# Kernel tuning notes

Measured on AMD Instinct MI355X. Metric: run time of the kernel, lower is better.

The kernel has to match this reference:

```python
import jax, jax.numpy as jnp
import numpy as np

EPSILON = 0.05


def _l2_normalize(x, axis=1, eps=1e-12):
    return x / jnp.maximum(jnp.linalg.norm(x, axis=axis, keepdims=True), eps)


def _pairwise_euclidean_distance(a, b):
    # [N, d], [K, d] -> [N, K] euclidean distances (torch.cdist semantics)
    sq = (jnp.sum(a * a, axis=1)[:, None]
          + jnp.sum(b * b, axis=1)[None, :]
          - 2.0 * (a @ b.T))
    return jnp.sqrt(jnp.maximum(sq, 1e-12))


def _sinkhorn(out, epsilon):
    # Faithful to the original: the loop body never updates Q, so the result
    # is a single row-then-column normalization regardless of `iterations`.
    Q = jnp.exp(out / epsilon).T              # [K, B]
    K, B = Q.shape
    Q = Q / jnp.sum(Q)
    Q1 = Q / jnp.sum(Q, axis=1, keepdims=True) / K
    Q2 = Q1 / jnp.sum(Q1, axis=0, keepdims=True) / B
    return (Q2 * B).T                          # [B, K]


def _cross_entropy(x1, x2):
    return -jnp.mean(jnp.sum(x1 * jnp.log(x2), axis=1))


def setup_inputs() -> dict:
    key = jax.random.key(0)
    k1, k2, k3 = jax.random.split(key, 3)
    two_bsz, d, K = 32768, 256, 1024
    return {
        "z": jax.random.normal(k1, (two_bsz, d), dtype=jnp.float32),
        "p": jax.random.normal(k2, (two_bsz, d), dtype=jnp.float32),
        "centers": jax.random.normal(k3, (K, d), dtype=jnp.float32),
    }


def reference(z, p, centers):
    z = _l2_normalize(z, axis=1)
    p = _l2_normalize(p, axis=1)
    c = _l2_normalize(centers, axis=1)

    bsz = z.shape[0] // 2
    z1, z2 = z[:bsz], z[bsz:]
    p1, p2 = p[:bsz], p[bsz:]

    za_1 = _sinkhorn(_pairwise_euclidean_distance(z1, c), EPSILON)
    za_2 = _sinkhorn(_pairwise_euclidean_distance(z2, c), EPSILON)
    pa_1 = _sinkhorn(_pairwise_euclidean_distance(p1, c), EPSILON)
    pa_2 = _sinkhorn(_pairwise_euclidean_distance(p2, c), EPSILON)

    # cls_use_both_views = True
    return (_cross_entropy(za_1, pa_1) + _cross_entropy(za_1, pa_2)
            + _cross_entropy(za_2, pa_1) + _cross_entropy(za_2, pa_2)) / 4.0
```

## Files before the change

kernel.cpp:

```cpp
#include <hip/hip_runtime.h>
#include <math.h>

#define BH  16384
#define B2  32768
#define DIM 256
#define KC  1024

typedef __bf16 bf16x8 __attribute__((ext_vector_type(8)));
typedef float  f32x4  __attribute__((ext_vector_type(4)));

__device__ __forceinline__ unsigned short f2bf(float f) {
  unsigned int u = __float_as_uint(f);
  u += 0x7FFFu + ((u >> 16) & 1u);
  return (unsigned short)(u >> 16);
}

__device__ __forceinline__ float vsqrt(float x) {
  float r; asm("v_sqrt_f32 %0, %1" : "=v"(r) : "v"(x)); return r;
}

__device__ __forceinline__ void gld_lds16(const void* g, void* l) {
  __builtin_amdgcn_global_load_lds(
      (const __attribute__((address_space(1))) void*)g,
      (__attribute__((address_space(3))) void*)l, 16, 0, 0);
}

__global__ void norm_rows_kernel(const float* __restrict__ z,
                                 const float* __restrict__ p,
                                 const float* __restrict__ c,
                                 unsigned short* __restrict__ Xn,
                                 unsigned short* __restrict__ Cn,
                                 float* __restrict__ colsum,
                                 float* __restrict__ out) {
  if (blockIdx.x < 16) colsum[blockIdx.x * 256 + threadIdx.x] = 0.0f;
  if (blockIdx.x == 16 && threadIdx.x == 0) out[0] = 0.0f;

  int wave = threadIdx.x >> 6;
  int lane = threadIdx.x & 63;
  int row  = blockIdx.x * 4 + wave;
  const float* src; unsigned short* dst; int r;
  if (row < B2)        { src = z; dst = Xn; r = row; }
  else if (row < 2*B2) { src = p; dst = Xn + (size_t)B2 * DIM; r = row - B2; }
  else                 { src = c; dst = Cn; r = row - 2*B2; }
  float4 v = *reinterpret_cast<const float4*>(src + (size_t)r * DIM + lane * 4);
  float ss = v.x*v.x + v.y*v.y + v.z*v.z + v.w*v.w;
  #pragma unroll
  for (int m = 1; m < 64; m <<= 1) ss += __shfl_xor(ss, m);
  float inv = 1.0f / fmaxf(vsqrt(ss), 1e-12f);
  ushort4 o;
  o.x = f2bf(v.x * inv); o.y = f2bf(v.y * inv);
  o.z = f2bf(v.z * inv); o.w = f2bf(v.w * inv);
  *reinterpret_cast<ushort4*>(dst + (size_t)r * DIM + lane * 4) = o;
}

__global__ void fin_logC_kernel(const float* __restrict__ colsum,
                                float* __restrict__ logC) {
  int i = blockIdx.x * 256 + threadIdx.x;
  if (i < 4 * KC) logC[i] = 40.0f + __logf(colsum[i]);
}

__global__ __launch_bounds__(256, 2)
void gemm_s_kernel(const unsigned short* __restrict__ XA,
                   const unsigned short* __restrict__ Cn,
                   float* __restrict__ colsum,
                   unsigned char* __restrict__ S) {
  __shared__ __align__(16) char lds[65536 + 4096];
  float* lut4 = (float*)(lds + 65536);
  const int id  = blockIdx.x;
  const int xcd = id & 7, idx = id >> 3;
  const int wk  = xcd * 128 + idx;
  const int panel = wk >> 3, col = wk & 7;
  const int tm0 = panel * 128, tn0 = col * 128;

  const int tid  = threadIdx.x;
  const int lane = tid & 63;
  const int wid  = tid >> 6;
  const int wm   = wid >> 1, wn = wid & 1;
  const int l15  = lane & 15, l4 = lane >> 4;
  const int slot = tid & 3;

  int arow[4], acs[4];
  #pragma unroll
  for (int it = 0; it < 4; ++it) {
    int sl = it * 256 + tid;
    int r = sl >> 3, c = sl & 7;
    arow[it] = r;
    acs[it]  = c ^ (r & 7);
  }
  const char* Abase = (const char*)XA + (size_t)tm0 * 512;
  const char* Bbase = (const char*)Cn + (size_t)tn0 * 512;

  auto stage = [&](int t) {
    const int mat = t >> 2;
    const int bk  = t & 3;
    const int b   = t & 1;
    const char* ab = Abase + ((size_t)mat << 23);
    #pragma unroll
    for (int it = 0; it < 4; ++it) {
      gld_lds16(ab + (size_t)arow[it] * 512 + bk * 128 + acs[it] * 16,
                lds + b * 16384 + (it * 256 + tid) * 16);
      gld_lds16(Bbase + (size_t)arow[it] * 512 + bk * 128 + acs[it] * 16,
                lds + 32768 + b * 16384 + (it * 256 + tid) * 16);
    }
  };

  if (tid < 256) {
    float d = ((float)tid - 127.5f) * (1.0f / 255.0f);
    float L = 20.0f * vsqrt(2.0f - 2.0f * d);
    float v = __expf(L - 40.0f);
    ((float4*)lut4)[tid] = (float4){v, v, v, v};
  }

  f32x4 acc[4][4];
  stage(0);
  __syncthreads();

  for (int t = 0; t < 16; ++t) {
    if (t < 15) stage(t + 1);
    const int b  = t & 1;
    const int mat = t >> 2, bk = t & 3;

    if (bk == 0) {
      #pragma unroll
      for (int fi = 0; fi < 4; ++fi)
        #pragma unroll
        for (int fj = 0; fj < 4; ++fj)
          acc[fi][fj] = (f32x4){0.f, 0.f, 0.f, 0.f};
    }

    #pragma unroll
    for (int kc = 0; kc < 2; ++kc) {
      bf16x8 aF[4], bF[4];
      #pragma unroll
      for (int f = 0; f < 4; ++f) {
        const int ra = wm * 64 + f * 16 + l15;
        aF[f] = *reinterpret_cast<const bf16x8*>(
            lds + b * 16384 + ra * 128 + ((((kc << 2) | l4) ^ (ra & 7)) << 4));
        const int rb = wn * 64 + f * 16 + l15;
        bF[f] = *reinterpret_cast<const bf16x8*>(
            lds + 32768 + b * 16384 + rb * 128 + ((((kc << 2) | l4) ^ (rb & 7)) << 4));
      }
      #pragma unroll
      for (int fi = 0; fi < 4; ++fi)
        #pragma unroll
        for (int fj = 0; fj < 4; ++fj)
          acc[fi][fj] = __builtin_amdgcn_mfma_f32_16x16x32_bf16(
              aF[fi], bF[fj], acc[fi][fj], 0, 0, 0);
    }

    if (bk == 3) {
      unsigned char* Sp = S + ((size_t)mat * BH + tm0) * KC + tn0;
      #pragma unroll
      for (int fj = 0; fj < 4; ++fj) {
        float cp = 0.0f;
        #pragma unroll
        for (int fi = 0; fi < 4; ++fi)
          #pragma unroll
          for (int i = 0; i < 4; ++i) {
            float v = fmaf(acc[fi][fj][i], 255.0f, 128.0f);
            v = fminf(fmaxf(v, 0.0f), 255.0f);
            unsigned e = (unsigned)v;
            cp += lut4[(e << 2) | slot];
            int row  = wm * 64 + fi * 16 + l4 * 4 + i;
            int ccol = wn * 64 + fj * 16 + l15;
            Sp[(size_t)row * KC + ccol] = (unsigned char)e;
          }
        cp += __shfl_xor(cp, 16);
        cp += __shfl_xor(cp, 32);
        if (l4 == 0)
          atomicAdd(&colsum[mat * KC + tn0 + wn * 64 + fj * 16 + l15], cp);
      }
    }
    __syncthreads();
  }
}

__device__ __forceinline__ float decG(unsigned e, float lc) {
  float d = fmaf((float)e, 1.0f / 255.0f, -0.5f);
  float L = 20.0f * vsqrt(fmaf(-2.0f, d, 2.0f));
  return L - lc;
}

__global__ __launch_bounds__(256)
void pass2_mem_kernel(const unsigned char* __restrict__ S,
                      const float* __restrict__ logC,
                      float* __restrict__ rowv) {
  const int tid  = threadIdx.x;
  const int lane = tid & 63;
  const int wid  = tid >> 6;
  const int row  = blockIdx.x * 4 + wid;
  const size_t plane = (size_t)BH * KC;
  const unsigned char* Sr = S + (size_t)row * KC;

  float dp1 = 0.f, dp2 = 0.f, dz1 = 0.f, dz2 = 0.f, nz1 = 0.f, nz2 = 0.f;

  #pragma unroll
  for (int it = 0; it < 2; ++it) {
    const int kb = it * 512 + lane * 8;
    uint2 vz1 = *reinterpret_cast<const uint2*>(Sr + 0 * plane + kb);
    uint2 vz2 = *reinterpret_cast<const uint2*>(Sr + 1 * plane + kb);
    uint2 vp1 = *reinterpret_cast<const uint2*>(Sr + 2 * plane + kb);
    uint2 vp2 = *reinterpret_cast<const uint2*>(Sr + 3 * plane + kb);

    float cz1[8], cz2[8], cp1[8], cp2[8];
    *reinterpret_cast<float4*>(&cz1[0]) = *reinterpret_cast<const float4*>(logC + 0 * KC + kb);
    *reinterpret_cast<float4*>(&cz1[4]) = *reinterpret_cast<const float4*>(logC + 0 * KC + kb + 4);
    *reinterpret_cast<float4*>(&cz2[0]) = *reinterpret_cast<const float4*>(logC + 1 * KC + kb);
    *reinterpret_cast<float4*>(&cz2[4]) = *reinterpret_cast<const float4*>(logC + 1 * KC + kb + 4);
    *reinterpret_cast<float4*>(&cp1[0]) = *reinterpret_cast<const float4*>(logC + 2 * KC + kb);
    *reinterpret_cast<float4*>(&cp1[4]) = *reinterpret_cast<const float4*>(logC + 2 * KC + kb + 4);
    *reinterpret_cast<float4*>(&cp2[0]) = *reinterpret_cast<const float4*>(logC + 3 * KC + kb);
    *reinterpret_cast<float4*>(&cp2[4]) = *reinterpret_cast<const float4*>(logC + 3 * KC + kb + 4);

    unsigned b1[8], b2[8];
    #pragma unroll
    for (int e = 0; e < 4; ++e) {
      b1[e]     = (vp1.x >> (8 * e)) & 0xffu;
      b1[e + 4] = (vp1.y >> (8 * e)) & 0xffu;
      b2[e]     = (vp2.x >> (8 * e)) & 0xffu;
      b2[e + 4] = (vp2.y >> (8 * e)) & 0xffu;
    }
    float tv[8];
    #pragma unroll
    for (int e = 0; e < 8; ++e) {
      float g1 = decG(b1[e], cp1[e]);
      float g2 = decG(b2[e], cp2[e]);
      dp1 += __expf(g1);
      dp2 += __expf(g2);
      tv[e] = g1 + g2;
    }
    #pragma unroll
    for (int e = 0; e < 4; ++e) {
      b1[e]     = (vz1.x >> (8 * e)) & 0xffu;
      b1[e + 4] = (vz1.y >> (8 * e)) & 0xffu;
      b2[e]     = (vz2.x >> (8 * e)) & 0xffu;
      b2[e + 4] = (vz2.y >> (8 * e)) & 0xffu;
    }
    #pragma unroll
    for (int e = 0; e < 8; ++e) {
      float e1 = __expf(decG(b1[e], cz1[e]));
      float e2 = __expf(decG(b2[e], cz2[e]));
      dz1 += e1; nz1 += e1 * tv[e];
      dz2 += e2; nz2 += e2 * tv[e];
    }
  }

  #pragma unroll
  for (int m = 1; m < 64; m <<= 1) {
    dp1 += __shfl_xor(dp1, m); dp2 += __shfl_xor(dp2, m);
    dz1 += __shfl_xor(dz1, m); dz2 += __shfl_xor(dz2, m);
    nz1 += __shfl_xor(nz1, m); nz2 += __shfl_xor(nz2, m);
  }

  __shared__ float red[4];
  if (lane == 0)
    red[wid] = nz1 / dz1 + nz2 / dz2 - 2.0f * (__logf(dp1) + __logf(dp2));
  __syncthreads();
  if (tid == 0)
    rowv[blockIdx.x] = red[0] + red[1] + red[2] + red[3];
}

__global__ void fin_reduce_kernel(const float* __restrict__ rowv,
                                  float* __restrict__ out) {
  int i = blockIdx.x * 256 + threadIdx.x;
  float v = rowv[i];
  #pragma unroll
  for (int m = 1; m < 64; m <<= 1) v += __shfl_xor(v, m);
  __shared__ float ws[4];
  int lane = threadIdx.x & 63, wid = threadIdx.x >> 6;
  if (lane == 0) ws[wid] = v;
  __syncthreads();
  if (threadIdx.x == 0)
    atomicAdd(out, (ws[0] + ws[1] + ws[2] + ws[3]) * (-1.0f / 65536.0f));
}

extern "C" void kernel_launch(void* const* d_in, const int* in_sizes, int n_in,
                              void* d_out, int out_size, void* d_ws, size_t ws_size,
                              hipStream_t stream) {
  const float* z = (const float*)d_in[0];
  const float* p = (const float*)d_in[1];
  const float* c = (const float*)d_in[2];
  char* ws = (char*)d_ws;
  unsigned short* Xn = (unsigned short*)(ws);
  unsigned short* Cn = (unsigned short*)(ws + 33554432);
  float* colsum = (float*)(ws + 34078720);
  float* logC   = (float*)(ws + 34095104);
  float* rowv   = (float*)(ws + 34111488);
  unsigned char* S = (unsigned char*)(ws + 34127872);
  float* out = (float*)d_out;

  norm_rows_kernel<<<16640, 256, 0, stream>>>(z, p, c, Xn, Cn, colsum, out);
  gemm_s_kernel<<<1024, 256, 0, stream>>>(Xn, Cn, colsum, S);
  fin_logC_kernel<<<16, 256, 0, stream>>>(colsum, logC);
  pass2_mem_kernel<<<4096, 256, 0, stream>>>(S, logC, rowv);
  fin_reduce_kernel<<<16, 256, 0, stream>>>(rowv, out);
}
```

Measured before the change: 107.8 us.

## Read center tiles directly from global memory and widen pass2 row loads

The GEMM kernel stops staging the centers (B) tile through LDS and loads B fragments straight from global memory into registers, halving the LDS footprint. This could raise occupancy and cut the LDS write and read traffic, at the cost of uncoalesced global reads that lack the swizzle and depend on cache hits. Separately, pass2 loads 16 bytes per lane per plane in one shot instead of two 8-byte iterations, which gives fewer, wider memory requests.

```diff
diff --git a/kernel.cpp b/kernel.cpp
--- a/kernel.cpp
+++ b/kernel.cpp
@@ -64,8 +64,8 @@
                    const unsigned short* __restrict__ Cn,
                    float* __restrict__ colsum,
                    unsigned char* __restrict__ S) {
-  __shared__ __align__(16) char lds[65536 + 4096];
-  float* lut4 = (float*)(lds + 65536);
+  __shared__ __align__(16) char lds[36864];
+  float* lut4 = (float*)(lds + 32768);
   const int id  = blockIdx.x;
   const int xcd = id & 7, idx = id >> 3;
   const int wk  = xcd * 128 + idx;
@@ -99,8 +99,6 @@
     for (int it = 0; it < 4; ++it) {
       gld_lds16(ab + (size_t)arow[it] * 512 + bk * 128 + acs[it] * 16,
                 lds + b * 16384 + (it * 256 + tid) * 16);
-      gld_lds16(Bbase + (size_t)arow[it] * 512 + bk * 128 + acs[it] * 16,
-                lds + 32768 + b * 16384 + (it * 256 + tid) * 16);
     }
   };
 
@@ -133,12 +131,12 @@
       bf16x8 aF[4], bF[4];
       #pragma unroll
       for (int f = 0; f < 4; ++f) {
+        const int rb = wn * 64 + f * 16 + l15;
+        bF[f] = *reinterpret_cast<const bf16x8*>(
+            Bbase + (size_t)rb * 512 + bk * 128 + ((kc << 2) | l4) * 16);
         const int ra = wm * 64 + f * 16 + l15;
         aF[f] = *reinterpret_cast<const bf16x8*>(
             lds + b * 16384 + ra * 128 + ((((kc << 2) | l4) ^ (ra & 7)) << 4));
-        const int rb = wn * 64 + f * 16 + l15;
-        bF[f] = *reinterpret_cast<const bf16x8*>(
-            lds + 32768 + b * 16384 + rb * 128 + ((((kc << 2) | l4) ^ (rb & 7)) << 4));
       }
       #pragma unroll
       for (int fi = 0; fi < 4; ++fi)
@@ -190,56 +188,56 @@
   const int wid  = tid >> 6;
   const int row  = blockIdx.x * 4 + wid;
   const size_t plane = (size_t)BH * KC;
-  const unsigned char* Sr = S + (size_t)row * KC;
+  const unsigned char* Sr = S + (size_t)row * KC + lane * 16;
+  const int kb = lane * 16;
+
+  uint4 vz1 = *reinterpret_cast<const uint4*>(Sr + 0 * plane);
+  uint4 vz2 = *reinterpret_cast<const uint4*>(Sr + 1 * plane);
+  uint4 vp1 = *reinterpret_cast<const uint4*>(Sr + 2 * plane);
+  uint4 vp2 = *reinterpret_cast<const uint4*>(Sr + 3 * plane);
 
   float dp1 = 0.f, dp2 = 0.f, dz1 = 0.f, dz2 = 0.f, nz1 = 0.f, nz2 = 0.f;
-
-  #pragma unroll
-  for (int it = 0; it < 2; ++it) {
-    const int kb = it * 512 + lane * 8;
-    uint2 vz1 = *reinterpret_cast<const uint2*>(Sr + 0 * plane + kb);
-    uint2 vz2 = *reinterpret_cast<const uint2*>(Sr + 1 * plane + kb);
-    uint2 vp1 = *reinterpret_cast<const uint2*>(Sr + 2 * plane + kb);
-    uint2 vp2 = *reinterpret_cast<const uint2*>(Sr + 3 * plane + kb);
-
-    float cz1[8], cz2[8], cp1[8], cp2[8];
-    *reinterpret_cast<float4*>(&cz1[0]) = *reinterpret_cast<const float4*>(logC + 0 * KC + kb);
-    *reinterpret_cast<float4*>(&cz1[4]) = *reinterpret_cast<const float4*>(logC + 0 * KC + kb + 4);
-    *reinterpret_cast<float4*>(&cz2[0]) = *reinterpret_cast<const float4*>(logC + 1 * KC + kb);
-    *reinterpret_cast<float4*>(&cz2[4]) = *reinterpret_cast<const float4*>(logC + 1 * KC + kb + 4);
-    *reinterpret_cast<float4*>(&cp1[0]) = *reinterpret_cast<const float4*>(logC + 2 * KC + kb);
-    *reinterpret_cast<float4*>(&cp1[4]) = *reinterpret_cast<const float4*>(logC + 2 * KC + kb + 4);
-    *reinterpret_cast<float4*>(&cp2[0]) = *reinterpret_cast<const float4*>(logC + 3 * KC + kb);
-    *reinterpret_cast<float4*>(&cp2[4]) = *reinterpret_cast<const float4*>(logC + 3 * KC + kb + 4);
-
-    unsigned b1[8], b2[8];
-    #pragma unroll
-    for (int e = 0; e < 4; ++e) {
-      b1[e]     = (vp1.x >> (8 * e)) & 0xffu;
-      b1[e + 4] = (vp1.y >> (8 * e)) & 0xffu;
-      b2[e]     = (vp2.x >> (8 * e)) & 0xffu;
-      b2[e + 4] = (vp2.y >> (8 * e)) & 0xffu;
-    }
-    float tv[8];
-    #pragma unroll
-    for (int e = 0; e < 8; ++e) {
-      float g1 = decG(b1[e], cp1[e]);
-      float g2 = decG(b2[e], cp2[e]);
+  float tv[16];
+
+  {
+    const unsigned w1[4] = {vp1.x, vp1.y, vp1.z, vp1.w};
+    const unsigned w2[4] = {vp2.x, vp2.y, vp2.z, vp2.w};
+    float lc1[16], lc2[16];
+    #pragma unroll
+    for (int q = 0; q < 4; ++q) {
+      *reinterpret_cast<float4*>(&lc1[q * 4]) =
+          *reinterpret_cast<const float4*>(logC + 2 * KC + kb + q * 4);
+      *reinterpret_cast<float4*>(&lc2[q * 4]) =
+          *reinterpret_cast<const float4*>(logC + 3 * KC + kb + q * 4);
+    }
+    #pragma unroll
+    for (int e = 0; e < 16; ++e) {
+      unsigned b1 = (w1[e >> 2] >> ((e & 3) * 8)) & 0xffu;
+      unsigned b2 = (w2[e >> 2] >> ((e & 3) * 8)) & 0xffu;
+      float g1 = decG(b1, lc1[e]);
+      float g2 = decG(b2, lc2[e]);
       dp1 += __expf(g1);
       dp2 += __expf(g2);
       tv[e] = g1 + g2;
     }
-    #pragma unroll
-    for (int e = 0; e < 4; ++e) {
-      b1[e]     = (vz1.x >> (8 * e)) & 0xffu;
-      b1[e + 4] = (vz1.y >> (8 * e)) & 0xffu;
-      b2[e]     = (vz2.x >> (8 * e)) & 0xffu;
-      b2[e + 4] = (vz2.y >> (8 * e)) & 0xffu;
-    }
-    #pragma unroll
-    for (int e = 0; e < 8; ++e) {
-      float e1 = __expf(decG(b1[e], cz1[e]));
-      float e2 = __expf(decG(b2[e], cz2[e]));
+  }
+  {
+    const unsigned w1[4] = {vz1.x, vz1.y, vz1.z, vz1.w};
+    const unsigned w2[4] = {vz2.x, vz2.y, vz2.z, vz2.w};
+    float lc1[16], lc2[16];
+    #pragma unroll
+    for (int q = 0; q < 4; ++q) {
+      *reinterpret_cast<float4*>(&lc1[q * 4]) =
+          *reinterpret_cast<const float4*>(logC + 0 * KC + kb + q * 4);
+      *reinterpret_cast<float4*>(&lc2[q * 4]) =
+          *reinterpret_cast<const float4*>(logC + 1 * KC + kb + q * 4);
+    }
+    #pragma unroll
+    for (int e = 0; e < 16; ++e) {
+      unsigned b1 = (w1[e >> 2] >> ((e & 3) * 8)) & 0xffu;
+      unsigned b2 = (w2[e >> 2] >> ((e & 3) * 8)) & 0xffu;
+      float e1 = __expf(decG(b1, lc1[e]));
+      float e2 = __expf(decG(b2, lc2[e]));
       dz1 += e1; nz1 += e1 * tv[e];
       dz2 += e2; nz2 += e2 * tv[e];
     }
```

Result: slower. 139.9 us (+29.8%).
